# Optimization experiments

Measured on AMD Instinct MI355X. Metric: run time of the kernel, lower is better.

The kernel has to match this reference:

```python
import jax, jax.numpy as jnp
import numpy as np

D_MODEL = 1024
NHEAD = 16
HEAD_DIM = D_MODEL // NHEAD
WINDOW = 33  # mask keeps |i-j| > WINDOW//2 (True = attend, matching torch SDPA bool-mask semantics)


def setup_inputs() -> dict:
    key = jax.random.key(0)
    ks = jax.random.split(key, 9)
    s = 1.0 / np.sqrt(D_MODEL)
    x = jax.random.normal(ks[0], (2, 2048, D_MODEL), dtype=jnp.float32)
    Wq = jax.random.uniform(ks[1], (D_MODEL, D_MODEL), jnp.float32, -s, s)
    bq = jax.random.uniform(ks[2], (D_MODEL,), jnp.float32, -s, s)
    Wk = jax.random.uniform(ks[3], (D_MODEL, D_MODEL), jnp.float32, -s, s)
    bk = jax.random.uniform(ks[4], (D_MODEL,), jnp.float32, -s, s)
    Wv = jax.random.uniform(ks[5], (D_MODEL, D_MODEL), jnp.float32, -s, s)
    bv = jax.random.uniform(ks[6], (D_MODEL,), jnp.float32, -s, s)
    Wo = jax.random.uniform(ks[7], (D_MODEL, D_MODEL), jnp.float32, -s, s)
    bo = jax.random.uniform(ks[8], (D_MODEL,), jnp.float32, -s, s)
    return {"x": x, "Wq": Wq, "bq": bq, "Wk": Wk, "bk": bk,
            "Wv": Wv, "bv": bv, "Wo": Wo, "bo": bo}


def reference(x, Wq, bq, Wk, bk, Wv, bv, Wo, bo):
    B, T, C = x.shape
    H, D = NHEAD, HEAD_DIM
    # projections (torch Linear: y = x @ W.T + b)
    q = (x @ Wq.T + bq).reshape(B, T, H, D).transpose(0, 2, 1, 3)  # [B,H,T,D]
    k = (x @ Wk.T + bk).reshape(B, T, H, D).transpose(0, 2, 1, 3)
    v = (x @ Wv.T + bv).reshape(B, T, H, D).transpose(0, 2, 1, 3)
    idx = jnp.arange(T)
    rel = jnp.abs(idx[:, None] - idx[None, :])
    keep = rel > (WINDOW // 2)  # True = participate (torch SDPA bool-mask semantics)
    scale = 1.0 / jnp.sqrt(jnp.asarray(D, dtype=x.dtype))
    scores = jnp.einsum('bhqd,bhkd->bhqk', q, k) * scale
    scores = jnp.where(keep, scores, jnp.asarray(-jnp.inf, dtype=scores.dtype))
    attn = jax.nn.softmax(scores, axis=-1)
    out = jnp.einsum('bhqk,bhkd->bhqd', attn, v)  # [B,H,T,D]
    out = out.transpose(0, 2, 1, 3).reshape(B, T, C)
    return out @ Wo.T + bo
```

## Files before the change

### kernel.cpp

```cpp
#include <hip/hip_runtime.h>
#include <stdint.h>


typedef unsigned short u16;
typedef short bf16x8 __attribute__((ext_vector_type(8)));
typedef float f32x4 __attribute__((ext_vector_type(4)));

#define MFMA16 __builtin_amdgcn_mfma_f32_16x16x32_bf16

__device__ __forceinline__ u16 f2bf(float f) {
  union { float f; uint32_t u; } v; v.f = f;
  return (u16)((v.u + 0x7fffu + ((v.u >> 16) & 1u)) >> 16);
}

__device__ __forceinline__ uint32_t cvt_pk_bf16(float lo, float hi) {
  uint32_t d;
  asm("v_cvt_pk_bf16_f32 %0, %1, %2" : "=v"(d) : "v"(lo), "v"(hi));
  return d;
}

__device__ __forceinline__ float hexp2(float x) {
  float r;
  asm("v_exp_f32 %0, %1" : "=v"(r) : "v"(x));
  return r;
}

__global__ void f2b5_kernel(const float* __restrict__ x,
                            const float* __restrict__ a, const float* __restrict__ b,
                            const float* __restrict__ c, const float* __restrict__ d,
                            u16* __restrict__ ox, u16* __restrict__ oa, u16* __restrict__ ob,
                            u16* __restrict__ oc, u16* __restrict__ od) {
  int bid = blockIdx.x;
  const float* src; u16* dst; int base;
  if (bid < 4096)      { src = x; dst = ox; base = 0; }
  else if (bid < 5120) { src = a; dst = oa; base = 4096; }
  else if (bid < 6144) { src = b; dst = ob; base = 5120; }
  else if (bid < 7168) { src = c; dst = oc; base = 6144; }
  else                 { src = d; dst = od; base = 7168; }
  int i = (bid - base) * 256 + threadIdx.x;
  float4 v = reinterpret_cast<const float4*>(src)[i];
  ushort4 o;
  o.x = f2bf(v.x); o.y = f2bf(v.y); o.z = f2bf(v.z); o.w = f2bf(v.w);
  reinterpret_cast<ushort4*>(dst)[i] = o;
}

#define GEMM_LOAD(REGA, REGB, A_, B_, KOFF)                                                        \
  do {                                                                                             \
    REGA##0 = *reinterpret_cast<const uint4*>(A_ + (size_t)(gm_base +  0) * 1024 + (KOFF) + sslot * 8); \
    REGA##1 = *reinterpret_cast<const uint4*>(A_ + (size_t)(gm_base + 32) * 1024 + (KOFF) + sslot * 8); \
    REGA##2 = *reinterpret_cast<const uint4*>(A_ + (size_t)(gm_base + 64) * 1024 + (KOFF) + sslot * 8); \
    REGA##3 = *reinterpret_cast<const uint4*>(A_ + (size_t)(gm_base + 96) * 1024 + (KOFF) + sslot * 8); \
    REGB##0 = *reinterpret_cast<const uint4*>(B_ + (size_t)(gn_base +  0) * 1024 + (KOFF) + sslot * 8); \
    REGB##1 = *reinterpret_cast<const uint4*>(B_ + (size_t)(gn_base + 32) * 1024 + (KOFF) + sslot * 8); \
    REGB##2 = *reinterpret_cast<const uint4*>(B_ + (size_t)(gn_base + 64) * 1024 + (KOFF) + sslot * 8); \
    REGB##3 = *reinterpret_cast<const uint4*>(B_ + (size_t)(gn_base + 96) * 1024 + (KOFF) + sslot * 8); \
  } while (0)

#define GEMM_PUBLISH()                                                                             \
  do {                                                                                             \
    *reinterpret_cast<uint4*>((char*)As + (srow +  0) * 144 + sslot * 16) = ar0;                   \
    *reinterpret_cast<uint4*>((char*)As + (srow + 32) * 144 + sslot * 16) = ar1;                   \
    *reinterpret_cast<uint4*>((char*)As + (srow + 64) * 144 + sslot * 16) = ar2;                   \
    *reinterpret_cast<uint4*>((char*)As + (srow + 96) * 144 + sslot * 16) = ar3;                   \
    *reinterpret_cast<uint4*>((char*)Bs + (srow +  0) * 144 + sslot * 16) = br0;                   \
    *reinterpret_cast<uint4*>((char*)Bs + (srow + 32) * 144 + sslot * 16) = br1;                   \
    *reinterpret_cast<uint4*>((char*)Bs + (srow + 64) * 144 + sslot * 16) = br2;                   \
    *reinterpret_cast<uint4*>((char*)Bs + (srow + 96) * 144 + sslot * 16) = br3;                   \
  } while (0)

#define GEMM_CORE(A_, B_, bm0_, bn0_)                                                              \
  constexpr int KP = 72;                                                                           \
  __shared__ __align__(16) u16 As[128 * KP];                                                       \
  __shared__ __align__(16) u16 Bs[128 * KP];                                                       \
  const int t = threadIdx.x;                                                                       \
  const int lane = t & 63;                                                                         \
  const int wv = t >> 6;                                                                           \
  const int wm = (wv >> 1) * 64;                                                                   \
  const int wn = (wv & 1) * 64;                                                                    \
  const int lg = lane >> 4;                                                                        \
  const int lr = lane & 15;                                                                        \
  const int srow = t >> 3;                                                                         \
  const int sslot = t & 7;                                                                         \
  const int gm_base = bm0_ + srow;                                                                 \
  const int gn_base = bn0_ + srow;                                                                 \
  uint4 ar0, ar1, ar2, ar3, br0, br1, br2, br3;                                                    \
  f32x4 acc[4][4];                                                                                 \
  for (int i = 0; i < 4; ++i)                                                                      \
    for (int j = 0; j < 4; ++j) acc[i][j] = (f32x4)0.0f;                                           \
  GEMM_LOAD(ar, br, A_, B_, 0);                                                                    \
  for (int k0 = 0; k0 < 1024; k0 += 64) {                                                          \
    GEMM_PUBLISH();                                                                                \
    __syncthreads();                                                                               \
    if (k0 + 64 < 1024) GEMM_LOAD(ar, br, A_, B_, k0 + 64);                                        \
    for (int kk = 0; kk < 2; ++kk) {                                                               \
      bf16x8 af[4], bfr[4];                                                                        \
      for (int i = 0; i < 4; ++i)                                                                  \
        af[i] = *reinterpret_cast<const bf16x8*>(&As[(wm + i * 16 + lr) * KP + kk * 32 + lg * 8]); \
      for (int j = 0; j < 4; ++j)                                                                  \
        bfr[j] = *reinterpret_cast<const bf16x8*>(&Bs[(wn + j * 16 + lr) * KP + kk * 32 + lg * 8]);\
      for (int i = 0; i < 4; ++i)                                                                  \
        for (int j = 0; j < 4; ++j)                                                                \
          acc[i][j] = MFMA16(af[i], bfr[j], acc[i][j], 0, 0, 0);                                   \
    }                                                                                              \
    __syncthreads();                                                                               \
  }

__global__ __launch_bounds__(256) void gemm_qkv(
    const u16* __restrict__ A,
    const u16* __restrict__ Wqb, const u16* __restrict__ Wkb, const u16* __restrict__ Wvb,
    const float* __restrict__ bqp, const float* __restrict__ bkp, const float* __restrict__ bvp,
    u16* __restrict__ qo, u16* __restrict__ ko, u16* __restrict__ vo)
{
  const int bid = blockIdx.x + gridDim.x * blockIdx.y;
  const int sid = (bid & 7) * 96 + (bid >> 3);
  const int bm0 = (sid / 24) * 128;
  const int jy = sid % 24;
  const int sel = jy >> 3;
  const int bn0 = (jy & 7) * 128;

  const u16* Bw = (sel == 0) ? Wqb : (sel == 1) ? Wkb : Wvb;
  const float* bias = (sel == 0) ? bqp : (sel == 1) ? bkp : bvp;
  const float scale = (sel == 0) ? 0.125f * 1.44269504f : 1.0f;

  GEMM_CORE(A, Bw, bm0, bn0)

  for (int j = 0; j < 4; ++j) {
    int gn = bn0 + wn + j * 16 + lr;
    float bv = bias[gn];
    for (int i = 0; i < 4; ++i) {
      for (int r = 0; r < 4; ++r) {
        int gm = bm0 + wm + i * 16 + lg * 4 + r;
        float val = (acc[i][j][r] + bv) * scale;
        int b = gm >> 11, tt = gm & 2047;
        int h = gn >> 6,  d = gn & 63;
        u16 o = f2bf(val);
        if (sel == 0)
          qo[((size_t)(b * 16 + h) * 2048 + tt) * 64 + d] = o;
        else if (sel == 1)
          ko[((size_t)(b * 16 + h) * 2048 + tt) * 64 + d] = o;
        else
          vo[((size_t)(b * 16 + h) * 64 + d) * 2048 + tt] = o;
      }
    }
  }
}

__global__ __launch_bounds__(256) void gemm_out(
    const u16* __restrict__ A, const u16* __restrict__ Bw,
    const float* __restrict__ bias, float* __restrict__ outp)
{
  const int bid = blockIdx.x + gridDim.x * blockIdx.y;
  const int sid = (bid & 7) * 32 + (bid >> 3);
  const int bm0 = (sid >> 3) * 128;
  const int bn0 = (sid & 7) * 128;

  GEMM_CORE(A, Bw, bm0, bn0)

  for (int j = 0; j < 4; ++j) {
    int gn = bn0 + wn + j * 16 + lr;
    float bv = bias[gn];
    for (int i = 0; i < 4; ++i)
      for (int r = 0; r < 4; ++r) {
        int gm = bm0 + wm + i * 16 + lg * 4 + r;
        outp[(size_t)gm * 1024 + gn] = acc[i][j][r] + bv;
      }
  }
}

__global__ __launch_bounds__(256, 2) void attn_kernel(
    const u16* __restrict__ qb, const u16* __restrict__ kb,
    const u16* __restrict__ vtb, u16* __restrict__ ab)
{
  constexpr int KP = 72;
  __shared__ __align__(16) u16 Kb[2][64 * KP];
  __shared__ __align__(16) u16 Vb[2][64 * KP];
  __shared__ __align__(16) u16 Pl[4][32 * 64];

  const int bid = blockIdx.x + gridDim.x * blockIdx.y;
  const int sid = (bid & 7) * 64 + (bid >> 3);
  const int bx = sid & 15;
  const int bh = sid >> 4;

  const int t = threadIdx.x;
  const int lane = t & 63;
  const int wv = t >> 6;
  const int lg = lane >> 4, lr = lane & 15;
  const int q0 = bx * 128 + wv * 32;

  const u16* Qp = qb + (size_t)bh * 2048 * 64;
  const u16* Kp = kb + (size_t)bh * 2048 * 64;
  const u16* Vt = vtb + (size_t)bh * 64 * 2048;
  char* Pw = (char*)&Pl[wv][0];
  const int swz = (lr & 7) << 4;

  const int sl = lane & 7;
  const int r0 = wv * 16 + (lane >> 3);
  const int sdst0 = r0 * (KP * 2) + sl * 16;

  uint4 krA, krB, vrA, vrB;

#define ISSUE_LOADS(J0N)                                                                 \
  do {                                                                                   \
    krA = *reinterpret_cast<const uint4*>(Kp + (size_t)((J0N) + r0) * 64 + sl * 8);      \
    krB = *reinterpret_cast<const uint4*>(Kp + (size_t)((J0N) + r0 + 8) * 64 + sl * 8);  \
    vrA = *reinterpret_cast<const uint4*>(Vt + (size_t)r0 * 2048 + (J0N) + sl * 8);      \
    vrB = *reinterpret_cast<const uint4*>(Vt + (size_t)(r0 + 8) * 2048 + (J0N) + sl * 8);\
  } while (0)

#define WRITE_LDS(BUF)                                                                   \
  do {                                                                                   \
    *reinterpret_cast<uint4*>((char*)&Kb[BUF][0] + sdst0)                = krA;          \
    *reinterpret_cast<uint4*>((char*)&Kb[BUF][0] + sdst0 + 8 * KP * 2)   = krB;          \
    *reinterpret_cast<uint4*>((char*)&Vb[BUF][0] + sdst0)                = vrA;          \
    *reinterpret_cast<uint4*>((char*)&Vb[BUF][0] + sdst0 + 8 * KP * 2)   = vrB;          \
  } while (0)

  bf16x8 qf[2][2];
  for (int qi = 0; qi < 2; ++qi)
    for (int h = 0; h < 2; ++h)
      qf[qi][h] = *reinterpret_cast<const bf16x8*>(&Qp[(size_t)(q0 + qi * 16 + lr) * 64 + h * 32 + lg * 8]);

  f32x4 o[2][4];
  for (int qi = 0; qi < 2; ++qi)
    for (int d = 0; d < 4; ++d) o[qi][d] = (f32x4)0.0f;
  float m[2] = {-1e30f, -1e30f};
  float lsum[2] = {0.0f, 0.0f};

  ISSUE_LOADS(0);
  WRITE_LDS(0);
  __syncthreads();
  int cur = 0;

  for (int tt = 0; tt < 32; ++tt) {
    if (tt < 31) ISSUE_LOADS((tt + 1) * 64);
    const int j0 = tt * 64;

    f32x4 s[2][4];
    __builtin_amdgcn_s_setprio(1);
    for (int kc = 0; kc < 4; ++kc) {
      bf16x8 kf0 = *reinterpret_cast<const bf16x8*>(&Kb[cur][(kc * 16 + lr) * KP + lg * 8]);
      bf16x8 kf1 = *reinterpret_cast<const bf16x8*>(&Kb[cur][(kc * 16 + lr) * KP + 32 + lg * 8]);
      for (int qi = 0; qi < 2; ++qi) {
        f32x4 z = (f32x4)0.0f;
        z = MFMA16(kf0, qf[qi][0], z, 0, 0, 0);
        z = MFMA16(kf1, qf[qi][1], z, 0, 0, 0);
        s[qi][kc] = z;
      }
    }
    __builtin_amdgcn_s_setprio(0);
    if (j0 + 63 >= q0 - 16 && j0 <= q0 + 47) {
      for (int qi = 0; qi < 2; ++qi)
        for (int kc = 0; kc < 4; ++kc)
          for (int r = 0; r < 4; ++r) {
            int i = q0 + qi * 16 + lr;
            int j = j0 + kc * 16 + lg * 4 + r;
            int dd = i - j; if (dd < 0) dd = -dd;
            if (dd <= 16) s[qi][kc][r] = -1e38f;
          }
    }
    float pm[2];
    for (int qi = 0; qi < 2; ++qi) {
      f32x4 t4 = __builtin_elementwise_max(__builtin_elementwise_max(s[qi][0], s[qi][1]),
                                           __builtin_elementwise_max(s[qi][2], s[qi][3]));
      float x = fmaxf(fmaxf(t4[0], t4[1]), fmaxf(t4[2], t4[3]));
      x = fmaxf(x, __shfl_xor(x, 16));
      x = fmaxf(x, __shfl_xor(x, 32));
      pm[qi] = x;
    }
    bool need = (pm[0] > m[0] + 11.54f) || (pm[1] > m[1] + 11.54f);
    if (__any((int)need)) {
      for (int qi = 0; qi < 2; ++qi) {
        float mn = fmaxf(m[qi], pm[qi]);
        float a = hexp2(m[qi] - mn);
        m[qi] = mn;
        lsum[qi] *= a;
        for (int d = 0; d < 4; ++d) o[qi][d] *= a;
      }
    }
    for (int qi = 0; qi < 2; ++qi) {
      int rowbase = (qi * 16 + lr) * 128;
      float psum = 0.0f;
      for (int kc = 0; kc < 4; ++kc) {
        float p0 = hexp2(s[qi][kc][0] - m[qi]);
        float p1 = hexp2(s[qi][kc][1] - m[qi]);
        float p2 = hexp2(s[qi][kc][2] - m[qi]);
        float p3 = hexp2(s[qi][kc][3] - m[qi]);
        psum += (p0 + p1) + (p2 + p3);
        uint2 pk;
        pk.x = cvt_pk_bf16(p0, p1);
        pk.y = cvt_pk_bf16(p2, p3);
        *reinterpret_cast<uint2*>(Pw + ((rowbase + kc * 32 + lg * 8) ^ swz)) = pk;
      }
      lsum[qi] += psum;
    }
    asm volatile("s_waitcnt lgkmcnt(0)" ::: "memory");
    __builtin_amdgcn_s_setprio(1);
    for (int kh = 0; kh < 2; ++kh) {
      bf16x8 pa[2];
      for (int qi = 0; qi < 2; ++qi)
        pa[qi] = *reinterpret_cast<const bf16x8*>(
            Pw + (((qi * 16 + lr) * 128 + kh * 64 + lg * 16) ^ swz));
      for (int d = 0; d < 4; ++d) {
        bf16x8 vf = *reinterpret_cast<const bf16x8*>(
            &Vb[cur][(d * 16 + lr) * KP + kh * 32 + lg * 8]);
        for (int qi = 0; qi < 2; ++qi)
          o[qi][d] = MFMA16(vf, pa[qi], o[qi][d], 0, 0, 0);
      }
    }
    __builtin_amdgcn_s_setprio(0);
    if (tt < 31) WRITE_LDS(cur ^ 1);
    __syncthreads();
    cur ^= 1;
  }

  int b = bh >> 4, h = bh & 15;
  for (int qi = 0; qi < 2; ++qi) {
    float ls = lsum[qi];
    ls += __shfl_xor(ls, 16);
    ls += __shfl_xor(ls, 32);
    float inv = 1.0f / ls;
    size_t rowoff = ((size_t)b * 2048 + q0 + qi * 16 + lr) * 1024 + h * 64;
    for (int d = 0; d < 4; ++d) {
      uint2 pk;
      pk.x = cvt_pk_bf16(o[qi][d][0] * inv, o[qi][d][1] * inv);
      pk.y = cvt_pk_bf16(o[qi][d][2] * inv, o[qi][d][3] * inv);
      *reinterpret_cast<uint2*>(&ab[rowoff + d * 16 + lg * 4]) = pk;
    }
  }
#undef ISSUE_LOADS
#undef WRITE_LDS
}

extern "C" void kernel_launch(void* const* d_in, const int* in_sizes, int n_in,
                              void* d_out, int out_size, void* d_ws, size_t ws_size,
                              hipStream_t stream) {
  const float* x  = (const float*)d_in[0];
  const float* Wq = (const float*)d_in[1];
  const float* bq = (const float*)d_in[2];
  const float* Wk = (const float*)d_in[3];
  const float* bk = (const float*)d_in[4];
  const float* Wv = (const float*)d_in[5];
  const float* bv = (const float*)d_in[6];
  const float* Wo = (const float*)d_in[7];
  const float* bo = (const float*)d_in[8];

  u16* ws  = (u16*)d_ws;
  u16* xb  = ws;
  u16* wqb = ws + 4194304;
  u16* wkb = ws + 5242880;
  u16* wvb = ws + 6291456;
  u16* wob = ws + 7340032;
  u16* qbf = ws + 8388608;
  u16* kbf = ws + 12582912;
  u16* vbf = ws + 16777216;
  u16* ab  = xb;

  f2b5_kernel<<<8192, 256, 0, stream>>>(x, Wq, Wk, Wv, Wo, xb, wqb, wkb, wvb, wob);

  gemm_qkv<<<dim3(32, 24), 256, 0, stream>>>(xb, wqb, wkb, wvb, bq, bk, bv, qbf, kbf, vbf);

  attn_kernel<<<dim3(16, 32), 256, 0, stream>>>(qbf, kbf, vbf, ab);

  gemm_out<<<dim3(32, 8), 256, 0, stream>>>(ab, wob, bo, (float*)d_out);
}
```

Baseline: 135.0 us.

## Fuse fp32-to-bf16 conversion into GEMM tile loads, drop separate cast kernel

Removes the standalone conversion kernel that turned x and all four weight matrices into bf16. The GEMMs now read fp32 directly from global memory and pack to bf16 with v_cvt_pk_bf16 before writing to LDS. This saves a launch and a full write-then-read of the bf16 copies. In exchange, each GEMM tile re-reads twice as many bytes from global memory per operand, repeated across every block that shares the operand, and needs more registers for staging.

Measured after the change: 142.7 us. 5.7% more time.

```diff
diff --git a/kernel.cpp b/kernel.cpp
--- a/kernel.cpp
+++ b/kernel.cpp
@@ -7,11 +7,6 @@
 typedef float f32x4 __attribute__((ext_vector_type(4)));
 
 #define MFMA16 __builtin_amdgcn_mfma_f32_16x16x32_bf16
-
-__device__ __forceinline__ u16 f2bf(float f) {
-  union { float f; uint32_t u; } v; v.f = f;
-  return (u16)((v.u + 0x7fffu + ((v.u >> 16) & 1u)) >> 16);
-}
 
 __device__ __forceinline__ uint32_t cvt_pk_bf16(float lo, float hi) {
   uint32_t d;
@@ -19,56 +14,18 @@
   return d;
 }
 
+__device__ __forceinline__ u16 f2bf(float f) {
+  union { float f; uint32_t u; } v; v.f = f;
+  return (u16)((v.u + 0x7fffu + ((v.u >> 16) & 1u)) >> 16);
+}
+
 __device__ __forceinline__ float hexp2(float x) {
   float r;
   asm("v_exp_f32 %0, %1" : "=v"(r) : "v"(x));
   return r;
 }
 
-__global__ void f2b5_kernel(const float* __restrict__ x,
-                            const float* __restrict__ a, const float* __restrict__ b,
-                            const float* __restrict__ c, const float* __restrict__ d,
-                            u16* __restrict__ ox, u16* __restrict__ oa, u16* __restrict__ ob,
-                            u16* __restrict__ oc, u16* __restrict__ od) {
-  int bid = blockIdx.x;
-  const float* src; u16* dst; int base;
-  if (bid < 4096)      { src = x; dst = ox; base = 0; }
-  else if (bid < 5120) { src = a; dst = oa; base = 4096; }
-  else if (bid < 6144) { src = b; dst = ob; base = 5120; }
-  else if (bid < 7168) { src = c; dst = oc; base = 6144; }
-  else                 { src = d; dst = od; base = 7168; }
-  int i = (bid - base) * 256 + threadIdx.x;
-  float4 v = reinterpret_cast<const float4*>(src)[i];
-  ushort4 o;
-  o.x = f2bf(v.x); o.y = f2bf(v.y); o.z = f2bf(v.z); o.w = f2bf(v.w);
-  reinterpret_cast<ushort4*>(dst)[i] = o;
-}
-
-#define GEMM_LOAD(REGA, REGB, A_, B_, KOFF)                                                        \
-  do {                                                                                             \
-    REGA##0 = *reinterpret_cast<const uint4*>(A_ + (size_t)(gm_base +  0) * 1024 + (KOFF) + sslot * 8); \
-    REGA##1 = *reinterpret_cast<const uint4*>(A_ + (size_t)(gm_base + 32) * 1024 + (KOFF) + sslot * 8); \
-    REGA##2 = *reinterpret_cast<const uint4*>(A_ + (size_t)(gm_base + 64) * 1024 + (KOFF) + sslot * 8); \
-    REGA##3 = *reinterpret_cast<const uint4*>(A_ + (size_t)(gm_base + 96) * 1024 + (KOFF) + sslot * 8); \
-    REGB##0 = *reinterpret_cast<const uint4*>(B_ + (size_t)(gn_base +  0) * 1024 + (KOFF) + sslot * 8); \
-    REGB##1 = *reinterpret_cast<const uint4*>(B_ + (size_t)(gn_base + 32) * 1024 + (KOFF) + sslot * 8); \
-    REGB##2 = *reinterpret_cast<const uint4*>(B_ + (size_t)(gn_base + 64) * 1024 + (KOFF) + sslot * 8); \
-    REGB##3 = *reinterpret_cast<const uint4*>(B_ + (size_t)(gn_base + 96) * 1024 + (KOFF) + sslot * 8); \
-  } while (0)
-
-#define GEMM_PUBLISH()                                                                             \
-  do {                                                                                             \
-    *reinterpret_cast<uint4*>((char*)As + (srow +  0) * 144 + sslot * 16) = ar0;                   \
-    *reinterpret_cast<uint4*>((char*)As + (srow + 32) * 144 + sslot * 16) = ar1;                   \
-    *reinterpret_cast<uint4*>((char*)As + (srow + 64) * 144 + sslot * 16) = ar2;                   \
-    *reinterpret_cast<uint4*>((char*)As + (srow + 96) * 144 + sslot * 16) = ar3;                   \
-    *reinterpret_cast<uint4*>((char*)Bs + (srow +  0) * 144 + sslot * 16) = br0;                   \
-    *reinterpret_cast<uint4*>((char*)Bs + (srow + 32) * 144 + sslot * 16) = br1;                   \
-    *reinterpret_cast<uint4*>((char*)Bs + (srow + 64) * 144 + sslot * 16) = br2;                   \
-    *reinterpret_cast<uint4*>((char*)Bs + (srow + 96) * 144 + sslot * 16) = br3;                   \
-  } while (0)
-
-#define GEMM_CORE(A_, B_, bm0_, bn0_)                                                              \
+#define DECL_COMMON(bm0_, bn0_)                                                                    \
   constexpr int KP = 72;                                                                           \
   __shared__ __align__(16) u16 As[128 * KP];                                                       \
   __shared__ __align__(16) u16 Bs[128 * KP];                                                       \
@@ -83,15 +40,26 @@
   const int sslot = t & 7;                                                                         \
   const int gm_base = bm0_ + srow;                                                                 \
   const int gn_base = bn0_ + srow;                                                                 \
-  uint4 ar0, ar1, ar2, ar3, br0, br1, br2, br3;                                                    \
   f32x4 acc[4][4];                                                                                 \
   for (int i = 0; i < 4; ++i)                                                                      \
-    for (int j = 0; j < 4; ++j) acc[i][j] = (f32x4)0.0f;                                           \
-  GEMM_LOAD(ar, br, A_, B_, 0);                                                                    \
-  for (int k0 = 0; k0 < 1024; k0 += 64) {                                                          \
-    GEMM_PUBLISH();                                                                                \
-    __syncthreads();                                                                               \
-    if (k0 + 64 < 1024) GEMM_LOAD(ar, br, A_, B_, k0 + 64);                                        \
+    for (int j = 0; j < 4; ++j) acc[i][j] = (f32x4)0.0f;
+
+#define LD1_F32(LO, HI, SRC, RBASE, KOFF)                                                          \
+  LO = *reinterpret_cast<const float4*>(SRC + (size_t)(RBASE) * 1024 + (KOFF) + sslot * 8);        \
+  HI = *reinterpret_cast<const float4*>(SRC + (size_t)(RBASE) * 1024 + (KOFF) + sslot * 8 + 4);
+
+#define PUB1_F32(LO, HI, DST, RBASE)                                                               \
+  { uint4 w_;                                                                                      \
+    w_.x = cvt_pk_bf16(LO.x, LO.y); w_.y = cvt_pk_bf16(LO.z, LO.w);                                \
+    w_.z = cvt_pk_bf16(HI.x, HI.y); w_.w = cvt_pk_bf16(HI.z, HI.w);                                \
+    *reinterpret_cast<uint4*>((char*)DST + (RBASE) * 144 + sslot * 16) = w_; }
+
+#define LD1_H(RG, SRC, RBASE, KOFF)                                                                \
+  RG = *reinterpret_cast<const uint4*>(SRC + (size_t)(RBASE) * 1024 + (KOFF) + sslot * 8);
+#define PUB1_H(RG, DST, RBASE)                                                                     \
+  *reinterpret_cast<uint4*>((char*)DST + (RBASE) * 144 + sslot * 16) = RG;
+
+#define GEMM_MFMA_BODY()                                                                           \
     for (int kk = 0; kk < 2; ++kk) {                                                               \
       bf16x8 af[4], bfr[4];                                                                        \
       for (int i = 0; i < 4; ++i)                                                                  \
@@ -101,13 +69,11 @@
       for (int i = 0; i < 4; ++i)                                                                  \
         for (int j = 0; j < 4; ++j)                                                                \
           acc[i][j] = MFMA16(af[i], bfr[j], acc[i][j], 0, 0, 0);                                   \
-    }                                                                                              \
-    __syncthreads();                                                                               \
-  }
+    }
 
 __global__ __launch_bounds__(256) void gemm_qkv(
-    const u16* __restrict__ A,
-    const u16* __restrict__ Wqb, const u16* __restrict__ Wkb, const u16* __restrict__ Wvb,
+    const float* __restrict__ A,
+    const float* __restrict__ Wq, const float* __restrict__ Wk, const float* __restrict__ Wv,
     const float* __restrict__ bqp, const float* __restrict__ bkp, const float* __restrict__ bvp,
     u16* __restrict__ qo, u16* __restrict__ ko, u16* __restrict__ vo)
 {
@@ -118,11 +84,39 @@
   const int sel = jy >> 3;
   const int bn0 = (jy & 7) * 128;
 
-  const u16* Bw = (sel == 0) ? Wqb : (sel == 1) ? Wkb : Wvb;
+  const float* Bw = (sel == 0) ? Wq : (sel == 1) ? Wk : Wv;
   const float* bias = (sel == 0) ? bqp : (sel == 1) ? bkp : bvp;
   const float scale = (sel == 0) ? 0.125f * 1.44269504f : 1.0f;
 
-  GEMM_CORE(A, Bw, bm0, bn0)
+  DECL_COMMON(bm0, bn0)
+  float4 a0l, a0h, a1l, a1h, a2l, a2h, a3l, a3h;
+  float4 b0l, b0h, b1l, b1h, b2l, b2h, b3l, b3h;
+
+#define LD_FF(KOFF)                                                                                \
+  do {                                                                                             \
+    LD1_F32(a0l, a0h, A,  gm_base +  0, KOFF) LD1_F32(a1l, a1h, A,  gm_base + 32, KOFF)            \
+    LD1_F32(a2l, a2h, A,  gm_base + 64, KOFF) LD1_F32(a3l, a3h, A,  gm_base + 96, KOFF)            \
+    LD1_F32(b0l, b0h, Bw, gn_base +  0, KOFF) LD1_F32(b1l, b1h, Bw, gn_base + 32, KOFF)            \
+    LD1_F32(b2l, b2h, Bw, gn_base + 64, KOFF) LD1_F32(b3l, b3h, Bw, gn_base + 96, KOFF)            \
+  } while (0)
+#define PUB_FF()                                                                                   \
+  do {                                                                                             \
+    PUB1_F32(a0l, a0h, As, srow +  0) PUB1_F32(a1l, a1h, As, srow + 32)                            \
+    PUB1_F32(a2l, a2h, As, srow + 64) PUB1_F32(a3l, a3h, As, srow + 96)                            \
+    PUB1_F32(b0l, b0h, Bs, srow +  0) PUB1_F32(b1l, b1h, Bs, srow + 32)                            \
+    PUB1_F32(b2l, b2h, Bs, srow + 64) PUB1_F32(b3l, b3h, Bs, srow + 96)                            \
+  } while (0)
+
+  LD_FF(0);
+  for (int k0 = 0; k0 < 1024; k0 += 64) {
+    PUB_FF();
+    __syncthreads();
+    if (k0 + 64 < 1024) LD_FF(k0 + 64);
+    GEMM_MFMA_BODY()
+    __syncthreads();
+  }
+#undef LD_FF
+#undef PUB_FF
 
   for (int j = 0; j < 4; ++j) {
     int gn = bn0 + wn + j * 16 + lr;
@@ -146,7 +140,7 @@
 }
 
 __global__ __launch_bounds__(256) void gemm_out(
-    const u16* __restrict__ A, const u16* __restrict__ Bw,
+    const u16* __restrict__ A, const float* __restrict__ Bw,
     const float* __restrict__ bias, float* __restrict__ outp)
 {
   const int bid = blockIdx.x + gridDim.x * blockIdx.y;
@@ -154,7 +148,35 @@
   const int bm0 = (sid >> 3) * 128;
   const int bn0 = (sid & 7) * 128;
 
-  GEMM_CORE(A, Bw, bm0, bn0)
+  DECL_COMMON(bm0, bn0)
+  uint4 ar0, ar1, ar2, ar3;
+  float4 b0l, b0h, b1l, b1h, b2l, b2h, b3l, b3h;
+
+#define LD_HF(KOFF)                                                                                \
+  do {                                                                                             \
+    LD1_H(ar0, A, gm_base +  0, KOFF) LD1_H(ar1, A, gm_base + 32, KOFF)                            \
+    LD1_H(ar2, A, gm_base + 64, KOFF) LD1_H(ar3, A, gm_base + 96, KOFF)                            \
+    LD1_F32(b0l, b0h, Bw, gn_base +  0, KOFF) LD1_F32(b1l, b1h, Bw, gn_base + 32, KOFF)            \
+    LD1_F32(b2l, b2h, Bw, gn_base + 64, KOFF) LD1_F32(b3l, b3h, Bw, gn_base + 96, KOFF)            \
+  } while (0)
+#define PUB_HF()                                                                                   \
+  do {                                                                                             \
+    PUB1_H(ar0, As, srow +  0) PUB1_H(ar1, As, srow + 32)                                          \
+    PUB1_H(ar2, As, srow + 64) PUB1_H(ar3, As, srow + 96)                                          \
+    PUB1_F32(b0l, b0h, Bs, srow +  0) PUB1_F32(b1l, b1h, Bs, srow + 32)                            \
+    PUB1_F32(b2l, b2h, Bs, srow + 64) PUB1_F32(b3l, b3h, Bs, srow + 96)                            \
+  } while (0)
+
+  LD_HF(0);
+  for (int k0 = 0; k0 < 1024; k0 += 64) {
+    PUB_HF();
+    __syncthreads();
+    if (k0 + 64 < 1024) LD_HF(k0 + 64);
+    GEMM_MFMA_BODY()
+    __syncthreads();
+  }
+#undef LD_HF
+#undef PUB_HF
 
   for (int j = 0; j < 4; ++j) {
     int gn = bn0 + wn + j * 16 + lr;
@@ -345,21 +367,14 @@
   const float* bo = (const float*)d_in[8];
 
   u16* ws  = (u16*)d_ws;
-  u16* xb  = ws;
-  u16* wqb = ws + 4194304;
-  u16* wkb = ws + 5242880;
-  u16* wvb = ws + 6291456;
-  u16* wob = ws + 7340032;
-  u16* qbf = ws + 8388608;
-  u16* kbf = ws + 12582912;
-  u16* vbf = ws + 16777216;
-  u16* ab  = xb;
-
-  f2b5_kernel<<<8192, 256, 0, stream>>>(x, Wq, Wk, Wv, Wo, xb, wqb, wkb, wvb, wob);
-
-  gemm_qkv<<<dim3(32, 24), 256, 0, stream>>>(xb, wqb, wkb, wvb, bq, bk, bv, qbf, kbf, vbf);
+  u16* ab  = ws;
+  u16* qbf = ws + 4194304;
+  u16* kbf = ws + 8388608;
+  u16* vbf = ws + 12582912;
+
+  gemm_qkv<<<dim3(32, 24), 256, 0, stream>>>(x, Wq, Wk, Wv, bq, bk, bv, qbf, kbf, vbf);
 
   attn_kernel<<<dim3(16, 32), 256, 0, stream>>>(qbf, kbf, vbf, ab);
 
-  gemm_out<<<dim3(32, 8), 256, 0, stream>>>(ab, wob, bo, (float*)d_out);
-}
+  gemm_out<<<dim3(32, 8), 256, 0, stream>>>(ab, Wo, bo, (float*)d_out);
+}
```
